# Optimization experiments

Measured on AMD Instinct MI355X. Metric: run time of the kernel, lower is better.

The kernel has to match this reference:

```python
import jax, jax.numpy as jnp
import numpy as np

B, S, E, H = 2, 2048, 1024, 16
D = E // H  # dim per head


def setup_inputs() -> dict:
    key = jax.random.key(0)
    ks = jax.random.split(key, 13)
    sc = 1.0 / np.sqrt(E)
    inp = {
        "query": jax.random.normal(ks[0], (B, S, E), jnp.float32),
        "key": jax.random.normal(ks[1], (B, S, E), jnp.float32),
        "value": jax.random.normal(ks[2], (B, S, E), jnp.float32),
        "mask": jax.random.randint(ks[3], (B, S, S), 0, 2, jnp.int32),
        "Wq": jax.random.normal(ks[4], (E, E), jnp.float32) * sc,
        "bq": jnp.zeros((E,), jnp.float32),
        "Wk": jax.random.normal(ks[5], (E, E), jnp.float32) * sc,
        "bk": jnp.zeros((E,), jnp.float32),
        "Wv": jax.random.normal(ks[6], (E, E), jnp.float32) * sc,
        "bv": jnp.zeros((E,), jnp.float32),
        "Wo": jax.random.normal(ks[7], (E, E), jnp.float32) * sc,
        "bo": jnp.zeros((E,), jnp.float32),
    }
    return inp


def _split_heads(x):
    # [B, S, E] -> [B, H, S, D]
    return x.reshape(B, S, H, D).transpose(0, 2, 1, 3)


def reference(query, key, value, mask, Wq, bq, Wk, bk, Wv, bv, Wo, bo):
    q = _split_heads(query @ Wq.T + bq)
    k = _split_heads(key @ Wk.T + bk)
    v = _split_heads(value @ Wv.T + bv)

    dk = k.shape[-1]
    # scores: [B, H, Sq, Sk]
    scores = jnp.einsum("bhqd,bhkd->bhqk", q / jnp.sqrt(jnp.asarray(dk, q.dtype)), k)
    # mask broadcast over heads: [B, 1, Sq, Sk]; masked positions get -1e9
    scores = jnp.where(mask[:, None, :, :] == 0, jnp.asarray(-1e9, scores.dtype), scores)
    # fp32 softmax (dropout is identity in eval mode)
    attn = jax.nn.softmax(scores.astype(jnp.float32), axis=-1).astype(q.dtype)
    out = jnp.einsum("bhqk,bhkd->bhqd", attn, v)
    out = out.transpose(0, 2, 1, 3).reshape(B, S, E)
    return out @ Wo.T + bo
```

## Files before the change

kernel.cpp:

```cpp
#include <hip/hip_runtime.h>
#include <hip/hip_bf16.h>
#include <stdint.h>


typedef __bf16 bf16x8 __attribute__((ext_vector_type(8)));
typedef __bf16 bf16x4 __attribute__((ext_vector_type(4)));
typedef float  f32x4  __attribute__((ext_vector_type(4)));
typedef unsigned int u32x4 __attribute__((ext_vector_type(4)));

#define MFMA16(a, b, c) __builtin_amdgcn_mfma_f32_16x16x32_bf16((a), (b), (c), 0, 0, 0)

#if __has_builtin(__builtin_amdgcn_exp2f)
#define EXP2(x) __builtin_amdgcn_exp2f(x)
#else
#define EXP2(x) exp2f(x)
#endif

static constexpr int kB = 2, kS = 2048, kE = 1024, kH = 16, kD = 64;
static constexpr int kM = kB * kS;
static constexpr int kMaskWordsPerRow = kS / 64;
static constexpr float kLog2e = 1.4426950408889634f;

__device__ __forceinline__ void gload_lds16(const void* g, void* l) {
  __builtin_amdgcn_global_load_lds(
      (const __attribute__((address_space(1))) unsigned int*)g,
      (__attribute__((address_space(3))) unsigned int*)l, 16, 0, 0);
}

__device__ __forceinline__ unsigned pack_bf16x2(float a, float b) {
  unsigned short lo = __builtin_bit_cast(unsigned short, (__bf16)a);
  unsigned short hi = __builtin_bit_cast(unsigned short, (__bf16)b);
  return (unsigned)lo | ((unsigned)hi << 16);
}

static constexpr int kCvtBlocks = 1664;

__global__ __launch_bounds__(256) void cvt_pack_kernel(
    const float* __restrict__ q, const float* __restrict__ k, const float* __restrict__ v,
    const float* __restrict__ wq, const float* __restrict__ wk,
    const float* __restrict__ wv, const float* __restrict__ wo,
    const int* __restrict__ mask,
    __bf16* __restrict__ qb, __bf16* __restrict__ kb, __bf16* __restrict__ vb,
    __bf16* __restrict__ wqb, __bf16* __restrict__ wkb,
    __bf16* __restrict__ wvb, __bf16* __restrict__ wob,
    unsigned long long* __restrict__ mw) {
  const int bid = blockIdx.x;
  if (bid < 1216) {
    const float* src; __bf16* dst; int n8, t0, stride;
    if (bid < 960) {
      const int seg = bid / 320, sb = bid - seg * 320;
      src = (seg == 0) ? q : (seg == 1) ? k : v;
      dst = (seg == 0) ? qb : (seg == 1) ? kb : vb;
      n8 = (kM * kE) >> 3;
      t0 = sb * 256 + threadIdx.x;
      stride = 320 * 256;
    } else {
      const int wseg = (bid - 960) >> 6, sb = (bid - 960) & 63;
      src = (wseg == 0) ? wq : (wseg == 1) ? wk : (wseg == 2) ? wv : wo;
      dst = (wseg == 0) ? wqb : (wseg == 1) ? wkb : (wseg == 2) ? wvb : wob;
      n8 = (kE * kE) >> 3;
      t0 = sb * 256 + threadIdx.x;
      stride = 64 * 256;
    }
    for (int i = t0; i < n8; i += stride) {
      float4 f0 = ((const float4*)src)[2 * i];
      float4 f1 = ((const float4*)src)[2 * i + 1];
      bf16x8 o = {(__bf16)f0.x, (__bf16)f0.y, (__bf16)f0.z, (__bf16)f0.w,
                  (__bf16)f1.x, (__bf16)f1.y, (__bf16)f1.z, (__bf16)f1.w};
      ((bf16x8*)dst)[i] = o;
    }
    return;
  }
  const int lane = threadIdx.x & 63;
  const int wid = ((bid - 1216) * 4 + (threadIdx.x >> 6));
  const int nwords = kB * kS * kMaskWordsPerRow;
  const int stride4 = 1792 * 4;
  for (int w = wid * 4; w < nwords; w += stride4) {
    const int v0 = mask[(size_t)(w + 0) * 64 + lane];
    const int v1 = mask[(size_t)(w + 1) * 64 + lane];
    const int v2 = mask[(size_t)(w + 2) * 64 + lane];
    const int v3 = mask[(size_t)(w + 3) * 64 + lane];
    const unsigned long long b0 = __ballot(v0 != 0);
    const unsigned long long b1 = __ballot(v1 != 0);
    const unsigned long long b2 = __ballot(v2 != 0);
    const unsigned long long b3 = __ballot(v3 != 0);
    if (lane == 0) {
      ulonglong2 lo = {b0, b1}, hi = {b2, b3};
      *(ulonglong2*)&mw[w] = lo;
      *(ulonglong2*)&mw[w + 2] = hi;
    }
  }
}

__global__ __launch_bounds__(256) void gemm_bt(
    const __bf16* __restrict__ A0, const __bf16* __restrict__ A1, const __bf16* __restrict__ A2,
    const __bf16* __restrict__ W0, const __bf16* __restrict__ W1, const __bf16* __restrict__ W2,
    const float* __restrict__ b0, const float* __restrict__ b1, const float* __restrict__ b2,
    __bf16* __restrict__ O0, __bf16* __restrict__ O1, __bf16* __restrict__ O2) {
  const int z = blockIdx.z;
  const __bf16* A = (z == 0) ? A0 : (z == 1) ? A1 : A2;
  const __bf16* W = (z == 0) ? W0 : (z == 1) ? W1 : W2;
  const float* bias = (z == 0) ? b0 : (z == 1) ? b1 : b2;
  __bf16* OutB = (z == 0) ? O0 : (z == 1) ? O1 : O2;
  const float scale = (z == 0) ? 0.125f * kLog2e : 1.0f;

  const int n0 = blockIdx.x * 128;
  const int m0 = blockIdx.y * 128;
  const int tid = threadIdx.x;
  const int wave = tid >> 6, lane = tid & 63;
  const int g = lane >> 4, qi = lane & 15;
  const int wm = wave >> 1, wn = wave & 1;

  __shared__ __align__(16) __bf16 As[128 * 32];
  __shared__ __align__(16) __bf16 Bs[128 * 32];
  __shared__ __align__(16) __bf16 Ts[64 * 136];

  f32x4 acc[4][4];
#pragma unroll
  for (int i = 0; i < 4; ++i)
#pragma unroll
    for (int jj = 0; jj < 4; ++jj) acc[i][jj] = (f32x4){0.f, 0.f, 0.f, 0.f};

  for (int k0 = 0; k0 < kE; k0 += 32) {
#pragma unroll
    for (int jj = 0; jj < 2; ++jj) {
      const int c = jj * 256 + tid;
      const int r = c >> 2, sl = c & 3;
      gload_lds16(&A[(size_t)(m0 + r) * kE + k0 + sl * 8], &As[c * 8]);
      gload_lds16(&W[(size_t)(n0 + r) * kE + k0 + sl * 8], &Bs[c * 8]);
    }
    __syncthreads();

    bf16x8 af[4], bfr[4];
#pragma unroll
    for (int mi = 0; mi < 4; ++mi)
      af[mi] = *(const bf16x8*)&As[(wm * 64 + mi * 16 + qi) * 32 + g * 8];
#pragma unroll
    for (int nj = 0; nj < 4; ++nj)
      bfr[nj] = *(const bf16x8*)&Bs[(wn * 64 + nj * 16 + qi) * 32 + g * 8];
#pragma unroll
    for (int mi = 0; mi < 4; ++mi)
#pragma unroll
      for (int nj = 0; nj < 4; ++nj)
        acc[mi][nj] = MFMA16(af[mi], bfr[nj], acc[mi][nj]);
    __syncthreads();
  }

  if (z == 2) {
    const int bb = m0 >> 11, ss0 = m0 & 2047;
#pragma unroll
    for (int half = 0; half < 2; ++half) {
      __syncthreads();
      if (wn == half) {
#pragma unroll
        for (int nj = 0; nj < 4; ++nj) {
          const int dl = nj * 16 + qi;
          const float bn = bias[n0 + half * 64 + dl];
#pragma unroll
          for (int mi = 0; mi < 4; ++mi) {
            const int srow = wm * 64 + mi * 16 + g * 4;
            bf16x4 o;
#pragma unroll
            for (int r = 0; r < 4; ++r) o[r] = (__bf16)(acc[mi][nj][r] + bn);
            *(bf16x4*)&Ts[dl * 136 + srow] = o;
          }
        }
      }
      __syncthreads();
      const int drow = tid >> 2, sc = (tid & 3) * 32;
      const int head = (n0 + half * 64) >> 6;
      __bf16* dst = OutB + (((size_t)bb * kH + head) * kD + drow) * kS + ss0 + sc;
#pragma unroll
      for (int jj = 0; jj < 4; ++jj) {
        bf16x8 vv = *(const bf16x8*)&Ts[drow * 136 + sc + jj * 8];
        *(bf16x8*)&dst[jj * 8] = vv;
      }
    }
    return;
  }

#pragma unroll
  for (int nj = 0; nj < 4; ++nj) {
    const int ncol = n0 + wn * 64 + nj * 16 + qi;
    const float bn = bias[ncol];
    const int hh = ncol >> 6, dd = ncol & 63;
#pragma unroll
    for (int mi = 0; mi < 4; ++mi) {
#pragma unroll
      for (int r = 0; r < 4; ++r) {
        const int mrow = m0 + wm * 64 + mi * 16 + g * 4 + r;
        const float vv = (acc[mi][nj][r] + bn) * scale;
        const int bb = mrow >> 11, ss = mrow & 2047;
        OutB[((((size_t)bb * kH + hh) * kS + ss) << 6) + dd] = (__bf16)vv;
      }
    }
  }
}

__global__ __launch_bounds__(256) void gemm_out64(
    const __bf16* __restrict__ A, const __bf16* __restrict__ W,
    const float* __restrict__ bias, float* __restrict__ OF) {
  const int n0 = blockIdx.x * 64;
  const int m0 = blockIdx.y * 128;
  const int tid = threadIdx.x;
  const int wave = tid >> 6, lane = tid & 63;
  const int g = lane >> 4, qi = lane & 15;
  const int wm = wave >> 1, wn = wave & 1;

  __shared__ __align__(16) __bf16 As[128 * 32];
  __shared__ __align__(16) __bf16 Bs[64 * 32];

  f32x4 acc[4][2];
#pragma unroll
  for (int i = 0; i < 4; ++i)
#pragma unroll
    for (int jj = 0; jj < 2; ++jj) acc[i][jj] = (f32x4){0.f, 0.f, 0.f, 0.f};

  for (int k0 = 0; k0 < kE; k0 += 32) {
#pragma unroll
    for (int jj = 0; jj < 2; ++jj) {
      const int c = jj * 256 + tid;
      const int r = c >> 2, sl = c & 3;
      gload_lds16(&A[(size_t)(m0 + r) * kE + k0 + sl * 8], &As[c * 8]);
    }
    {
      const int r = tid >> 2, sl = tid & 3;
      gload_lds16(&W[(size_t)(n0 + r) * kE + k0 + sl * 8], &Bs[tid * 8]);
    }
    __syncthreads();

    bf16x8 af[4], bfr[2];
#pragma unroll
    for (int mi = 0; mi < 4; ++mi)
      af[mi] = *(const bf16x8*)&As[(wm * 64 + mi * 16 + qi) * 32 + g * 8];
#pragma unroll
    for (int nj = 0; nj < 2; ++nj)
      bfr[nj] = *(const bf16x8*)&Bs[(wn * 32 + nj * 16 + qi) * 32 + g * 8];
#pragma unroll
    for (int mi = 0; mi < 4; ++mi)
#pragma unroll
      for (int nj = 0; nj < 2; ++nj)
        acc[mi][nj] = MFMA16(af[mi], bfr[nj], acc[mi][nj]);
    __syncthreads();
  }

#pragma unroll
  for (int nj = 0; nj < 2; ++nj) {
    const int ncol = n0 + wn * 32 + nj * 16 + qi;
    const float bn = bias[ncol];
#pragma unroll
    for (int mi = 0; mi < 4; ++mi)
#pragma unroll
      for (int r = 0; r < 4; ++r) {
        const int mrow = m0 + wm * 64 + mi * 16 + g * 4 + r;
        OF[(size_t)mrow * kE + ncol] = acc[mi][nj][r] + bn;
      }
  }
}

__global__ __launch_bounds__(512, 4) void attn_kernel(
    const __bf16* __restrict__ Qh, const __bf16* __restrict__ Kh,
    const __bf16* __restrict__ Vt, const unsigned long long* __restrict__ mw,
    __bf16* __restrict__ Ob) {
  const int tid = threadIdx.x;
  const int wave = tid >> 6, lane = tid & 63;
  const int g = lane >> 4, qi = lane & 15;
  const int id = blockIdx.x;
  const int xcd = id & 7, j = id >> 3;
  const int bh = xcd * 4 + (j >> 4);
  const int qb = j & 15;
  const int b = bh >> 4, h = bh & 15;

  __shared__ __align__(16) __bf16 Ks[2][128 * 64];
  __shared__ __align__(16) __bf16 Vs[2][64 * 128];

  const __bf16* Qp = Qh + (size_t)bh * kS * kD;
  const __bf16* Kp = Kh + (size_t)bh * kS * kD;
  const __bf16* Vp = Vt + (size_t)bh * kD * kS;

  const int q0 = qb * 128 + wave * 16 + qi;
  const unsigned long long* M0 = mw + (size_t)(b * kS + q0) * kMaskWordsPerRow;

  const bf16x8 qf0 = *(const bf16x8*)&Qp[(size_t)q0 * kD + g * 8];
  const bf16x8 qf1 = *(const bf16x8*)&Qp[(size_t)q0 * kD + 32 + g * 8];

  f32x4 acc[4];
#pragma unroll
  for (int f = 0; f < 4; ++f) acc[f] = (f32x4){0.f, 0.f, 0.f, 0.f};
  float den = 0.f;
  const float ninf = __builtin_bit_cast(float, 0xff800000u);

  auto stage = [&](int buf, int kv0) {
#pragma unroll
    for (int jj = 0; jj < 2; ++jj) {
      const int c = jj * 512 + tid;
      const int kr = c >> 3, ksl = c & 7;
      gload_lds16(&Kp[(size_t)(kv0 + kr) * kD + (ksl ^ (kr & 7)) * 8],
                  &Ks[buf][c * 8]);
      const int vr = c >> 4, vsl = c & 15;
      gload_lds16(&Vp[(size_t)vr * kS + kv0 + (vsl ^ (vr & 7)) * 8],
                  &Vs[buf][c * 8]);
    }
  };

  stage(0, 0);
  __syncthreads();

  const int sw = qi & 7;
  for (int t = 0; t < 16; ++t) {
    const int cur = t & 1;
    if (t < 15) stage(cur ^ 1, (t + 1) * 128);
    const ulonglong2 wpair = *(const ulonglong2*)&M0[2 * t];
#pragma unroll
    for (int u = 0; u < 2; ++u) {
      const unsigned long long w = u ? wpair.y : wpair.x;
      const unsigned wlo = (unsigned)(w >> (g * 4));
      const unsigned whi = (unsigned)(w >> (32 + g * 4));
      const unsigned wf[4] = {wlo, wlo >> 16, whi, whi >> 16};

      float p[16];
      __builtin_amdgcn_s_setprio(1);
#pragma unroll
      for (int f = 0; f < 4; ++f) {
        const int r = u * 64 + f * 16 + qi;
        const bf16x8 k0 = *(const bf16x8*)&Ks[cur][r * 64 + ((g ^ sw) * 8)];
        const bf16x8 k1 = *(const bf16x8*)&Ks[cur][r * 64 + (((4 + g) ^ sw) * 8)];
        f32x4 st = (f32x4){0.f, 0.f, 0.f, 0.f};
        st = MFMA16(k0, qf0, st);
        st = MFMA16(k1, qf1, st);
#pragma unroll
        for (int r4 = 0; r4 < 4; ++r4)
          p[4 * f + r4] = (wf[f] & (1u << r4)) ? st[r4] : ninf;
      }
      __builtin_amdgcn_s_setprio(0);

#pragma unroll
      for (int i = 0; i < 16; ++i) {
        p[i] = EXP2(p[i]);
        den += p[i];
      }

      unsigned pk[4][2];
#pragma unroll
      for (int f = 0; f < 4; ++f) {
        pk[f][0] = pack_bf16x2(p[4 * f + 0], p[4 * f + 1]);
        pk[f][1] = pack_bf16x2(p[4 * f + 2], p[4 * f + 3]);
      }
#pragma unroll
      for (int c = 0; c < 2; ++c) {
        unsigned bw[4];
#pragma unroll
        for (int t4 = 0; t4 < 4; ++t4) {
          const int src = qi + 16 * ((t4 >> 1) + 2 * (g & 1));
          const int vA = __shfl((int)pk[2 * c + 0][t4 & 1], src);
          const int vB = __shfl((int)pk[2 * c + 1][t4 & 1], src);
          bw[t4] = (g >= 2) ? (unsigned)vB : (unsigned)vA;
        }
        const u32x4 tmp = {bw[0], bw[1], bw[2], bw[3]};
        const bf16x8 pb = __builtin_bit_cast(bf16x8, tmp);
        __builtin_amdgcn_s_setprio(1);
#pragma unroll
        for (int f = 0; f < 4; ++f) {
          const int rd = f * 16 + qi;
          const int slot = (u * 8 + c * 4 + g) ^ sw;
          const bf16x8 vfr = *(const bf16x8*)&Vs[cur][rd * 128 + slot * 8];
          acc[f] = MFMA16(vfr, pb, acc[f]);
        }
        __builtin_amdgcn_s_setprio(0);
      }
    }
    __syncthreads();
  }

  den += __shfl_xor(den, 16);
  den += __shfl_xor(den, 32);
  const float rinv = 1.0f / den;
  __bf16* Op = Ob + (size_t)(b * kS + q0) * kE + h * kD;
#pragma unroll
  for (int f = 0; f < 4; ++f) {
    ushort4 o;
    o.x = __builtin_bit_cast(unsigned short, (__bf16)(acc[f][0] * rinv));
    o.y = __builtin_bit_cast(unsigned short, (__bf16)(acc[f][1] * rinv));
    o.z = __builtin_bit_cast(unsigned short, (__bf16)(acc[f][2] * rinv));
    o.w = __builtin_bit_cast(unsigned short, (__bf16)(acc[f][3] * rinv));
    *(ushort4*)&Op[f * 16 + g * 4] = o;
  }
}

extern "C" void kernel_launch(void* const* d_in, const int* in_sizes, int n_in,
                              void* d_out, int out_size, void* d_ws, size_t ws_size,
                              hipStream_t stream) {
  (void)in_sizes; (void)n_in; (void)out_size; (void)ws_size;
  const float* q  = (const float*)d_in[0];
  const float* k  = (const float*)d_in[1];
  const float* v  = (const float*)d_in[2];
  const int*   mask = (const int*)d_in[3];
  const float* Wq = (const float*)d_in[4];
  const float* bq = (const float*)d_in[5];
  const float* Wk = (const float*)d_in[6];
  const float* bk = (const float*)d_in[7];
  const float* Wv = (const float*)d_in[8];
  const float* bv = (const float*)d_in[9];
  const float* Wo = (const float*)d_in[10];
  const float* bo = (const float*)d_in[11];

  char* ws = (char*)d_ws;
  const size_t MB = 1024 * 1024;
  __bf16* qb  = (__bf16*)(ws + 0 * MB);
  __bf16* kb  = (__bf16*)(ws + 8 * MB);
  __bf16* vb  = (__bf16*)(ws + 16 * MB);
  __bf16* wqb = (__bf16*)(ws + 24 * MB);
  __bf16* wkb = (__bf16*)(ws + 26 * MB);
  __bf16* wvb = (__bf16*)(ws + 28 * MB);
  __bf16* wob = (__bf16*)(ws + 30 * MB);
  __bf16* Qh  = (__bf16*)(ws + 32 * MB);
  __bf16* Kh  = (__bf16*)(ws + 40 * MB);
  __bf16* Vt  = (__bf16*)(ws + 48 * MB);
  unsigned long long* mwords = (unsigned long long*)(ws + 56 * MB);
  __bf16* Ob = qb;

  cvt_pack_kernel<<<kCvtBlocks, 256, 0, stream>>>(
      q, k, v, Wq, Wk, Wv, Wo, mask, qb, kb, vb, wqb, wkb, wvb, wob, mwords);
  gemm_bt<<<dim3(8, 32, 3), 256, 0, stream>>>(qb, kb, vb, wqb, wkb, wvb,
                                              bq, bk, bv, Qh, Kh, Vt);
  attn_kernel<<<512, 512, 0, stream>>>(Qh, Kh, Vt, mwords, Ob);
  gemm_out64<<<dim3(16, 32), 256, 0, stream>>>(Ob, wob, bo, (float*)d_out);
}
```

Measured before the change: 285.9 us.

## Restructure attention into split-KV waves with direct global loads and MFMA row sums

The attention kernel is rebuilt with 256-thread blocks. Each wave handles two 16-row query tiles and one half of the KV range, and the two KV halves are merged through LDS at the end. K and V are read straight from global memory instead of being double-buffered in LDS, and the softmax denominator is computed with an MFMA against a ones vector rather than scalar adds. Separately, the Q/K GEMM epilogue now stages its output through LDS so head-layout stores are coalesced. The aim is more query reuse per K/V load and fewer barriers, at the risk of relying on the cache for K/V traffic.

```diff
diff --git a/kernel.cpp b/kernel.cpp
--- a/kernel.cpp
+++ b/kernel.cpp
@@ -113,7 +113,7 @@
 
   __shared__ __align__(16) __bf16 As[128 * 32];
   __shared__ __align__(16) __bf16 Bs[128 * 32];
-  __shared__ __align__(16) __bf16 Ts[64 * 136];
+  __shared__ __align__(16) __bf16 Ts[128 * 72];
 
   f32x4 acc[4][4];
 #pragma unroll
@@ -146,8 +146,8 @@
     __syncthreads();
   }
 
+  const int bb = m0 >> 11, ss0 = m0 & 2047;
   if (z == 2) {
-    const int bb = m0 >> 11, ss0 = m0 & 2047;
 #pragma unroll
     for (int half = 0; half < 2; ++half) {
       __syncthreads();
@@ -180,20 +180,30 @@
   }
 
 #pragma unroll
-  for (int nj = 0; nj < 4; ++nj) {
-    const int ncol = n0 + wn * 64 + nj * 16 + qi;
-    const float bn = bias[ncol];
-    const int hh = ncol >> 6, dd = ncol & 63;
-#pragma unroll
-    for (int mi = 0; mi < 4; ++mi) {
-#pragma unroll
-      for (int r = 0; r < 4; ++r) {
-        const int mrow = m0 + wm * 64 + mi * 16 + g * 4 + r;
-        const float vv = (acc[mi][nj][r] + bn) * scale;
-        const int bb = mrow >> 11, ss = mrow & 2047;
-        OutB[((((size_t)bb * kH + hh) * kS + ss) << 6) + dd] = (__bf16)vv;
-      }
-    }
+  for (int half = 0; half < 2; ++half) {
+    __syncthreads();
+    if (wn == half) {
+#pragma unroll
+      for (int nj = 0; nj < 4; ++nj) {
+        const int dl = nj * 16 + qi;
+        const float bn = bias[n0 + half * 64 + dl];
+#pragma unroll
+        for (int mi = 0; mi < 4; ++mi) {
+          const int srow = wm * 64 + mi * 16 + g * 4;
+#pragma unroll
+          for (int r = 0; r < 4; ++r)
+            Ts[(srow + r) * 72 + dl] = (__bf16)((acc[mi][nj][r] + bn) * scale);
+        }
+      }
+    }
+    __syncthreads();
+    const int row = tid >> 1, cg = tid & 1;
+    const int head = (n0 + half * 64) >> 6;
+    __bf16* dst =
+        OutB + (((size_t)bb * kH + head) * kS + ss0 + row) * kD + cg * 32;
+#pragma unroll
+    for (int jj = 0; jj < 4; ++jj)
+      *(bf16x8*)&dst[jj * 8] = *(const bf16x8*)&Ts[row * 72 + cg * 32 + jj * 8];
   }
 }
 
@@ -258,132 +268,164 @@
   }
 }
 
-__global__ __launch_bounds__(512, 4) void attn_kernel(
+__global__ __launch_bounds__(256, 4) void attn_kernel(
     const __bf16* __restrict__ Qh, const __bf16* __restrict__ Kh,
     const __bf16* __restrict__ Vt, const unsigned long long* __restrict__ mw,
     __bf16* __restrict__ Ob) {
   const int tid = threadIdx.x;
   const int wave = tid >> 6, lane = tid & 63;
   const int g = lane >> 4, qi = lane & 15;
+  const int qg = wave >> 1, kh = wave & 1;
   const int id = blockIdx.x;
   const int xcd = id & 7, j = id >> 3;
-  const int bh = xcd * 4 + (j >> 4);
-  const int qb = j & 15;
+  const int bh = xcd * 4 + (j >> 5);
+  const int qb = j & 31;
   const int b = bh >> 4, h = bh & 15;
-
-  __shared__ __align__(16) __bf16 Ks[2][128 * 64];
-  __shared__ __align__(16) __bf16 Vs[2][64 * 128];
 
   const __bf16* Qp = Qh + (size_t)bh * kS * kD;
   const __bf16* Kp = Kh + (size_t)bh * kS * kD;
   const __bf16* Vp = Vt + (size_t)bh * kD * kS;
 
-  const int q0 = qb * 128 + wave * 16 + qi;
-  const unsigned long long* M0 = mw + (size_t)(b * kS + q0) * kMaskWordsPerRow;
-
-  const bf16x8 qf0 = *(const bf16x8*)&Qp[(size_t)q0 * kD + g * 8];
-  const bf16x8 qf1 = *(const bf16x8*)&Qp[(size_t)q0 * kD + 32 + g * 8];
-
-  f32x4 acc[4];
-#pragma unroll
-  for (int f = 0; f < 4; ++f) acc[f] = (f32x4){0.f, 0.f, 0.f, 0.f};
-  float den = 0.f;
+  const int q0 = qb * 64 + qg * 32 + qi;
+  const int q1 = q0 + 16;
+  const int kvbase = kh * 1024;
+  const unsigned long long* M0 =
+      mw + (size_t)(b * kS + q0) * kMaskWordsPerRow + kh * 16;
+  const unsigned long long* M1 =
+      mw + (size_t)(b * kS + q1) * kMaskWordsPerRow + kh * 16;
+
+  const bf16x8 qf00 = *(const bf16x8*)&Qp[(size_t)q0 * kD + g * 8];
+  const bf16x8 qf01 = *(const bf16x8*)&Qp[(size_t)q0 * kD + 32 + g * 8];
+  const bf16x8 qf10 = *(const bf16x8*)&Qp[(size_t)q1 * kD + g * 8];
+  const bf16x8 qf11 = *(const bf16x8*)&Qp[(size_t)q1 * kD + 32 + g * 8];
+
+  f32x4 acc0[4], acc1[4];
+#pragma unroll
+  for (int f = 0; f < 4; ++f) {
+    acc0[f] = (f32x4){0.f, 0.f, 0.f, 0.f};
+    acc1[f] = (f32x4){0.f, 0.f, 0.f, 0.f};
+  }
+  f32x4 accd0 = (f32x4){0.f, 0.f, 0.f, 0.f};
+  f32x4 accd1 = (f32x4){0.f, 0.f, 0.f, 0.f};
+  const f32x4 kZero = (f32x4){0.f, 0.f, 0.f, 0.f};
   const float ninf = __builtin_bit_cast(float, 0xff800000u);
-
-  auto stage = [&](int buf, int kv0) {
-#pragma unroll
-    for (int jj = 0; jj < 2; ++jj) {
-      const int c = jj * 512 + tid;
-      const int kr = c >> 3, ksl = c & 7;
-      gload_lds16(&Kp[(size_t)(kv0 + kr) * kD + (ksl ^ (kr & 7)) * 8],
-                  &Ks[buf][c * 8]);
-      const int vr = c >> 4, vsl = c & 15;
-      gload_lds16(&Vp[(size_t)vr * kS + kv0 + (vsl ^ (vr & 7)) * 8],
-                  &Vs[buf][c * 8]);
-    }
-  };
-
-  stage(0, 0);
+  const u32x4 onesu = {0x3F803F80u, 0x3F803F80u, 0x3F803F80u, 0x3F803F80u};
+  const bf16x8 vones = __builtin_bit_cast(bf16x8, onesu);
+
+#pragma unroll 1
+  for (int t = 0; t < 16; ++t) {
+    const int kv0 = kvbase + t * 64;
+    const unsigned long long w0_ = M0[t], w1_ = M1[t];
+    unsigned wf0[4], wf1[4];
+    {
+      const unsigned lo0 = (unsigned)(w0_ >> (g * 4));
+      const unsigned hi0 = (unsigned)(w0_ >> (32 + g * 4));
+      wf0[0] = lo0; wf0[1] = lo0 >> 16; wf0[2] = hi0; wf0[3] = hi0 >> 16;
+      const unsigned lo1 = (unsigned)(w1_ >> (g * 4));
+      const unsigned hi1 = (unsigned)(w1_ >> (32 + g * 4));
+      wf1[0] = lo1; wf1[1] = lo1 >> 16; wf1[2] = hi1; wf1[3] = hi1 >> 16;
+    }
+
+    float p0[16], p1[16];
+    __builtin_amdgcn_s_setprio(1);
+#pragma unroll
+    for (int f = 0; f < 4; ++f) {
+      const __bf16* kr = &Kp[(size_t)(kv0 + f * 16 + qi) * kD];
+      const bf16x8 k0_ = *(const bf16x8*)&kr[g * 8];
+      const bf16x8 k1_ = *(const bf16x8*)&kr[32 + g * 8];
+      f32x4 st0 = MFMA16(k0_, qf00, kZero);
+      st0 = MFMA16(k1_, qf01, st0);
+      f32x4 st1 = MFMA16(k0_, qf10, kZero);
+      st1 = MFMA16(k1_, qf11, st1);
+#pragma unroll
+      for (int r4 = 0; r4 < 4; ++r4) {
+        p0[4 * f + r4] = (wf0[f] & (1u << r4)) ? st0[r4] : ninf;
+        p1[4 * f + r4] = (wf1[f] & (1u << r4)) ? st1[r4] : ninf;
+      }
+    }
+    __builtin_amdgcn_s_setprio(0);
+
+#pragma unroll
+    for (int i = 0; i < 16; ++i) {
+      p0[i] = EXP2(p0[i]);
+      p1[i] = EXP2(p1[i]);
+    }
+
+    unsigned pk0[4][2], pk1[4][2];
+#pragma unroll
+    for (int f = 0; f < 4; ++f) {
+      pk0[f][0] = pack_bf16x2(p0[4 * f + 0], p0[4 * f + 1]);
+      pk0[f][1] = pack_bf16x2(p0[4 * f + 2], p0[4 * f + 3]);
+      pk1[f][0] = pack_bf16x2(p1[4 * f + 0], p1[4 * f + 1]);
+      pk1[f][1] = pack_bf16x2(p1[4 * f + 2], p1[4 * f + 3]);
+    }
+#pragma unroll
+    for (int c = 0; c < 2; ++c) {
+      unsigned bw0[4], bw1[4];
+#pragma unroll
+      for (int t4 = 0; t4 < 4; ++t4) {
+        const int src_ = qi + 16 * ((t4 >> 1) + 2 * (g & 1));
+        const int a0_ = __shfl((int)pk0[2 * c + 0][t4 & 1], src_);
+        const int b0_ = __shfl((int)pk0[2 * c + 1][t4 & 1], src_);
+        bw0[t4] = (g >= 2) ? (unsigned)b0_ : (unsigned)a0_;
+        const int a1_ = __shfl((int)pk1[2 * c + 0][t4 & 1], src_);
+        const int b1_ = __shfl((int)pk1[2 * c + 1][t4 & 1], src_);
+        bw1[t4] = (g >= 2) ? (unsigned)b1_ : (unsigned)a1_;
+      }
+      const u32x4 u0_ = {bw0[0], bw0[1], bw0[2], bw0[3]};
+      const u32x4 u1_ = {bw1[0], bw1[1], bw1[2], bw1[3]};
+      const bf16x8 pb0 = __builtin_bit_cast(bf16x8, u0_);
+      const bf16x8 pb1 = __builtin_bit_cast(bf16x8, u1_);
+      __builtin_amdgcn_s_setprio(1);
+#pragma unroll
+      for (int f = 0; f < 4; ++f) {
+        const bf16x8 vf_ =
+            *(const bf16x8*)&Vp[(size_t)(f * 16 + qi) * kS + kv0 + c * 32 + g * 8];
+        acc0[f] = MFMA16(vf_, pb0, acc0[f]);
+        acc1[f] = MFMA16(vf_, pb1, acc1[f]);
+      }
+      accd0 = MFMA16(vones, pb0, accd0);
+      accd1 = MFMA16(vones, pb1, accd1);
+      __builtin_amdgcn_s_setprio(0);
+    }
+  }
+
+  __shared__ float rbuf[2][64][33];
+  __shared__ float rden[2][32];
+  if (kh == 1) {
+#pragma unroll
+    for (int f = 0; f < 4; ++f)
+#pragma unroll
+      for (int r = 0; r < 4; ++r) {
+        const int d = f * 16 + g * 4 + r;
+        rbuf[qg][d][qi] = acc0[f][r];
+        rbuf[qg][d][16 + qi] = acc1[f][r];
+      }
+    if (g == 0) {
+      rden[qg][qi] = accd0[0];
+      rden[qg][16 + qi] = accd1[0];
+    }
+  }
   __syncthreads();
-
-  const int sw = qi & 7;
-  for (int t = 0; t < 16; ++t) {
-    const int cur = t & 1;
-    if (t < 15) stage(cur ^ 1, (t + 1) * 128);
-    const ulonglong2 wpair = *(const ulonglong2*)&M0[2 * t];
-#pragma unroll
-    for (int u = 0; u < 2; ++u) {
-      const unsigned long long w = u ? wpair.y : wpair.x;
-      const unsigned wlo = (unsigned)(w >> (g * 4));
-      const unsigned whi = (unsigned)(w >> (32 + g * 4));
-      const unsigned wf[4] = {wlo, wlo >> 16, whi, whi >> 16};
-
-      float p[16];
-      __builtin_amdgcn_s_setprio(1);
-#pragma unroll
-      for (int f = 0; f < 4; ++f) {
-        const int r = u * 64 + f * 16 + qi;
-        const bf16x8 k0 = *(const bf16x8*)&Ks[cur][r * 64 + ((g ^ sw) * 8)];
-        const bf16x8 k1 = *(const bf16x8*)&Ks[cur][r * 64 + (((4 + g) ^ sw) * 8)];
-        f32x4 st = (f32x4){0.f, 0.f, 0.f, 0.f};
-        st = MFMA16(k0, qf0, st);
-        st = MFMA16(k1, qf1, st);
-#pragma unroll
-        for (int r4 = 0; r4 < 4; ++r4)
-          p[4 * f + r4] = (wf[f] & (1u << r4)) ? st[r4] : ninf;
-      }
-      __builtin_amdgcn_s_setprio(0);
-
-#pragma unroll
-      for (int i = 0; i < 16; ++i) {
-        p[i] = EXP2(p[i]);
-        den += p[i];
-      }
-
-      unsigned pk[4][2];
-#pragma unroll
-      for (int f = 0; f < 4; ++f) {
-        pk[f][0] = pack_bf16x2(p[4 * f + 0], p[4 * f + 1]);
-        pk[f][1] = pack_bf16x2(p[4 * f + 2], p[4 * f + 3]);
-      }
-#pragma unroll
-      for (int c = 0; c < 2; ++c) {
-        unsigned bw[4];
-#pragma unroll
-        for (int t4 = 0; t4 < 4; ++t4) {
-          const int src = qi + 16 * ((t4 >> 1) + 2 * (g & 1));
-          const int vA = __shfl((int)pk[2 * c + 0][t4 & 1], src);
-          const int vB = __shfl((int)pk[2 * c + 1][t4 & 1], src);
-          bw[t4] = (g >= 2) ? (unsigned)vB : (unsigned)vA;
-        }
-        const u32x4 tmp = {bw[0], bw[1], bw[2], bw[3]};
-        const bf16x8 pb = __builtin_bit_cast(bf16x8, tmp);
-        __builtin_amdgcn_s_setprio(1);
-#pragma unroll
-        for (int f = 0; f < 4; ++f) {
-          const int rd = f * 16 + qi;
-          const int slot = (u * 8 + c * 4 + g) ^ sw;
-          const bf16x8 vfr = *(const bf16x8*)&Vs[cur][rd * 128 + slot * 8];
-          acc[f] = MFMA16(vfr, pb, acc[f]);
-        }
-        __builtin_amdgcn_s_setprio(0);
-      }
-    }
-    __syncthreads();
-  }
-
-  den += __shfl_xor(den, 16);
-  den += __shfl_xor(den, 32);
-  const float rinv = 1.0f / den;
-  __bf16* Op = Ob + (size_t)(b * kS + q0) * kE + h * kD;
-#pragma unroll
-  for (int f = 0; f < 4; ++f) {
-    ushort4 o;
-    o.x = __builtin_bit_cast(unsigned short, (__bf16)(acc[f][0] * rinv));
-    o.y = __builtin_bit_cast(unsigned short, (__bf16)(acc[f][1] * rinv));
-    o.z = __builtin_bit_cast(unsigned short, (__bf16)(acc[f][2] * rinv));
-    o.w = __builtin_bit_cast(unsigned short, (__bf16)(acc[f][3] * rinv));
-    *(ushort4*)&Op[f * 16 + g * 4] = o;
+  if (kh == 0) {
+    const float ri0 = 1.0f / (accd0[0] + rden[qg][qi]);
+    const float ri1 = 1.0f / (accd1[0] + rden[qg][16 + qi]);
+    __bf16* Op0 = Ob + (size_t)(b * kS + q0) * kE + h * kD;
+    __bf16* Op1 = Ob + (size_t)(b * kS + q1) * kE + h * kD;
+#pragma unroll
+    for (int f = 0; f < 4; ++f) {
+      ushort4 o0, o1;
+#pragma unroll
+      for (int r = 0; r < 4; ++r) {
+        const int d = f * 16 + g * 4 + r;
+        const float v0 = (acc0[f][r] + rbuf[qg][d][qi]) * ri0;
+        const float v1 = (acc1[f][r] + rbuf[qg][d][16 + qi]) * ri1;
+        ((unsigned short*)&o0)[r] = __builtin_bit_cast(unsigned short, (__bf16)v0);
+        ((unsigned short*)&o1)[r] = __builtin_bit_cast(unsigned short, (__bf16)v1);
+      }
+      *(ushort4*)&Op0[f * 16 + g * 4] = o0;
+      *(ushort4*)&Op1[f * 16 + g * 4] = o1;
+    }
   }
 }
 
@@ -423,6 +465,6 @@
       q, k, v, Wq, Wk, Wv, Wo, mask, qb, kb, vb, wqb, wkb, wvb, wob, mwords);
   gemm_bt<<<dim3(8, 32, 3), 256, 0, stream>>>(qb, kb, vb, wqb, wkb, wvb,
                                               bq, bk, bv, Qh, Kh, Vt);
-  attn_kernel<<<512, 512, 0, stream>>>(Qh, Kh, Vt, mwords, Ob);
+  attn_kernel<<<1024, 256, 0, stream>>>(Qh, Kh, Vt, mwords, Ob);
   gemm_out64<<<dim3(16, 32), 256, 0, stream>>>(Ob, wob, bo, (float*)d_out);
 }
```

After: 344.5 us. 20.5% more time.
